# Kernel tuning notes

Measured on AMD Instinct MI355X. Metric: run time of the kernel, lower is better.

## Reference

```python
import jax, jax.numpy as jnp
import numpy as np

B, TQ, TK, D = 16, 2048, 2048, 128


def setup_inputs() -> dict:
    key = jax.random.key(0)
    kq, kk, kv, km = jax.random.split(key, 4)
    query = jax.random.normal(kq, (B, TQ, D), dtype=jnp.float32)
    key_t = jax.random.normal(kk, (B, TK, D), dtype=jnp.float32)
    value = jax.random.normal(kv, (B, TK, D), dtype=jnp.float32)
    mask = (jax.random.uniform(km, (B, TQ, TK)) > 0.9).astype(jnp.float32)
    return {"query": query, "key": key_t, "value": value, "mask": mask}


def reference(query, key, value, mask):
    # score = Q K^T / sqrt(dk)
    dk = jnp.asarray(query.shape[-1], query.dtype)
    score = jnp.einsum("bqd,bkd->bqk", query, key) / jnp.sqrt(dk)
    score = score + mask * (-10000.0)
    # NOTE: original code applies softmax over axis=1 (the query axis),
    # not the usual last axis; reproduced faithfully.
    attn_weights = jax.nn.softmax(score, axis=1)
    context = jnp.einsum("bqk,bkv->bqv", attn_weights, value)
    return context, attn_weights
```

## Files before the change

kernel.cpp:

```cpp
#include <hip/hip_runtime.h>

typedef __attribute__((ext_vector_type(8))) short s8v;
typedef __attribute__((ext_vector_type(4))) float f4v;

constexpr int BN = 16;
constexpr int TQ = 2048;
constexpr int TK = 2048;
constexpr int DH = 128;

__device__ __forceinline__ unsigned short f2bf(float f) {
  unsigned int u = __float_as_uint(f);
  u += 0x7fffu + ((u >> 16) & 1u);
  return (unsigned short)(u >> 16);
}
__device__ __forceinline__ float bf2f(unsigned short h) {
  return __uint_as_float(((unsigned int)h) << 16);
}

union QKSH {
  struct {
    unsigned short qhi[128][40];
    unsigned short qlo[128][40];
    unsigned short khi[128][40];
    unsigned short klo[128][40];
  } s;
  unsigned short msk[128][132];
};

__global__ __launch_bounds__(256, 4) void qk_exp_kernel(
    const float* __restrict__ Q, const float* __restrict__ K,
    const float* __restrict__ Msk, float* __restrict__ P,
    float* __restrict__ Z)
{
  __shared__ QKSH sh;

  const int kb = blockIdx.x, qb = blockIdx.y, b = blockIdx.z;
  const int tid = threadIdx.x;
  const int wave = tid >> 6, lane = tid & 63;
  const int wr = wave >> 1, wc = wave & 1;
  const int quad = lane >> 4, l16 = lane & 15;

  f4v acc[4][4];
#pragma unroll
  for (int i = 0; i < 4; ++i)
#pragma unroll
    for (int j = 0; j < 4; ++j)
      acc[i][j] = (f4v){0.f, 0.f, 0.f, 0.f};

  const float* Qb = Q + ((size_t)b * TQ + (size_t)qb * 128) * DH;
  const float* Kb = K + ((size_t)b * TK + (size_t)kb * 128) * DH;

  for (int dc = 0; dc < DH; dc += 32) {
    __syncthreads();
#pragma unroll
    for (int i = 0; i < 4; ++i) {
      int idx = i * 256 + tid;
      int r = idx >> 3, c = (idx & 7) * 4;
      float4 qv = *(const float4*)(Qb + (size_t)r * DH + dc + c);
      float4 kv = *(const float4*)(Kb + (size_t)r * DH + dc + c);
      unsigned short h;
      h = f2bf(qv.x); sh.s.qhi[r][c+0] = h; sh.s.qlo[r][c+0] = f2bf(qv.x - bf2f(h));
      h = f2bf(qv.y); sh.s.qhi[r][c+1] = h; sh.s.qlo[r][c+1] = f2bf(qv.y - bf2f(h));
      h = f2bf(qv.z); sh.s.qhi[r][c+2] = h; sh.s.qlo[r][c+2] = f2bf(qv.z - bf2f(h));
      h = f2bf(qv.w); sh.s.qhi[r][c+3] = h; sh.s.qlo[r][c+3] = f2bf(qv.w - bf2f(h));
      h = f2bf(kv.x); sh.s.khi[r][c+0] = h; sh.s.klo[r][c+0] = f2bf(kv.x - bf2f(h));
      h = f2bf(kv.y); sh.s.khi[r][c+1] = h; sh.s.klo[r][c+1] = f2bf(kv.y - bf2f(h));
      h = f2bf(kv.z); sh.s.khi[r][c+2] = h; sh.s.klo[r][c+2] = f2bf(kv.z - bf2f(h));
      h = f2bf(kv.w); sh.s.khi[r][c+3] = h; sh.s.klo[r][c+3] = f2bf(kv.w - bf2f(h));
    }
    __syncthreads();

    s8v ah[4], al[4];
#pragma unroll
    for (int i = 0; i < 4; ++i) {
      ah[i] = *(const s8v*)&sh.s.qhi[wr*64 + i*16 + l16][quad*8];
      al[i] = *(const s8v*)&sh.s.qlo[wr*64 + i*16 + l16][quad*8];
    }
#pragma unroll
    for (int j = 0; j < 4; ++j) {
      s8v bh = *(const s8v*)&sh.s.khi[wc*64 + j*16 + l16][quad*8];
      s8v bl = *(const s8v*)&sh.s.klo[wc*64 + j*16 + l16][quad*8];
#pragma unroll
      for (int i = 0; i < 4; ++i) {
        acc[i][j] = __builtin_amdgcn_mfma_f32_16x16x32_bf16(ah[i], bh, acc[i][j], 0, 0, 0);
        acc[i][j] = __builtin_amdgcn_mfma_f32_16x16x32_bf16(al[i], bh, acc[i][j], 0, 0, 0);
        acc[i][j] = __builtin_amdgcn_mfma_f32_16x16x32_bf16(ah[i], bl, acc[i][j], 0, 0, 0);
      }
    }
  }

  __syncthreads();
  {
    const float* MB = Msk + ((size_t)b * TQ + (size_t)qb * 128) * TK + (size_t)kb * 128;
#pragma unroll
    for (int it = 0; it < 16; ++it) {
      int idx = it * 256 + tid;
      int r = idx >> 5, c = (idx & 31) * 4;
      float4 mv = *(const float4*)(MB + (size_t)r * TK + c);
      ushort4 mu;
      mu.x = (mv.x != 0.f); mu.y = (mv.y != 0.f);
      mu.z = (mv.z != 0.f); mu.w = (mv.w != 0.f);
      *(ushort4*)&sh.msk[r][c] = mu;
    }
  }
  __syncthreads();

  const float scale = 0.08838834764831845f;
  float csum[4] = {0.f, 0.f, 0.f, 0.f};
#pragma unroll
  for (int i = 0; i < 4; ++i) {
    int lr0 = wr * 64 + i * 16 + quad * 4;
#pragma unroll
    for (int r = 0; r < 4; ++r) {
      size_t rowoff = ((size_t)b * TQ + qb * 128 + lr0 + r) * TK + kb * 128 + wc * 64;
      const unsigned short* mrow = &sh.msk[lr0 + r][wc * 64];
#pragma unroll
      for (int j = 0; j < 4; ++j) {
        unsigned short m = mrow[j * 16 + l16];
        float p = m ? 0.f : __expf(acc[i][j][r] * scale);
        P[rowoff + j * 16 + l16] = p;
        csum[j] += p;
      }
    }
  }
#pragma unroll
  for (int j = 0; j < 4; ++j) {
    float v = csum[j];
    v += __shfl_xor(v, 16, 64);
    v += __shfl_xor(v, 32, 64);
    if (quad == 0)
      atomicAdd(&Z[b * TK + kb * 128 + wc * 64 + j * 16 + l16], v);
  }
}

__global__ __launch_bounds__(256) void vtrans_kernel(
    const float* __restrict__ V, unsigned short* __restrict__ Vthi,
    unsigned short* __restrict__ Vtlo)
{
  __shared__ float tile[64][65];
  const int k0 = blockIdx.x * 64, d0 = blockIdx.y * 64, b = blockIdx.z;
  const int tid = threadIdx.x;
#pragma unroll
  for (int i = 0; i < 4; ++i) {
    int idx = i * 256 + tid;
    int r = idx >> 4, c = (idx & 15) * 4;
    float4 v = *(const float4*)(V + ((size_t)b * TK + k0 + r) * DH + d0 + c);
    tile[r][c] = v.x; tile[r][c+1] = v.y; tile[r][c+2] = v.z; tile[r][c+3] = v.w;
  }
  __syncthreads();
  const int dr = tid >> 2, kq = (tid & 3) * 16;
  size_t base = ((size_t)b * DH + d0 + dr) * TK + k0 + kq;
  unsigned short hbuf[16], lbuf[16];
#pragma unroll
  for (int j = 0; j < 16; ++j) {
    float f = tile[kq + j][dr];
    unsigned short h = f2bf(f);
    hbuf[j] = h;
    lbuf[j] = f2bf(f - bf2f(h));
  }
#pragma unroll
  for (int m = 0; m < 4; ++m) {
    ushort4 hv = make_ushort4(hbuf[4*m], hbuf[4*m+1], hbuf[4*m+2], hbuf[4*m+3]);
    ushort4 lv = make_ushort4(lbuf[4*m], lbuf[4*m+1], lbuf[4*m+2], lbuf[4*m+3]);
    *(ushort4*)(Vthi + base + 4*m) = hv;
    *(ushort4*)(Vtlo + base + 4*m) = lv;
  }
}

__global__ __launch_bounds__(256) void rz_kernel(const float* __restrict__ Z,
                                                 float* __restrict__ Rz) {
  int i = blockIdx.x * 256 + threadIdx.x;
  Rz[i] = 1.0f / Z[i];
}

union __align__(16) AVSH {
  struct {
    unsigned short a[64][40];
    unsigned short vh[128][40];
    unsigned short vl[128][40];
  } b[2];
  float ctx[64][131];
};

__global__ __launch_bounds__(256) void av_kernel(
    float* __restrict__ Attn, const unsigned short* __restrict__ Vthi,
    const unsigned short* __restrict__ Vtlo, const float* __restrict__ Rz,
    float* __restrict__ Ctx)
{
  __shared__ AVSH sh;
  const int qb = blockIdx.x, b = blockIdx.y;
  const int tid = threadIdx.x;
  const int wave = tid >> 6, lane = tid & 63;
  const int wr = wave >> 1, wc = wave & 1;
  const int quad = lane >> 4, l16 = lane & 15;

  f4v acc[4][2];
#pragma unroll
  for (int i = 0; i < 4; ++i)
#pragma unroll
    for (int j = 0; j < 2; ++j)
      acc[i][j] = (f4v){0.f, 0.f, 0.f, 0.f};

  float* attnB = Attn + ((size_t)b * TQ + (size_t)qb * 64) * TK;
  const unsigned short* vhB = Vthi + (size_t)b * DH * TK;
  const unsigned short* vlB = Vtlo + (size_t)b * DH * TK;
  const float* rzB = Rz + (size_t)b * TK;

  const int pc = (tid & 7) * 4;
  const int pr = tid >> 3;
  const int vc = (tid & 3) * 8;
  const int vr = tid >> 2;

  float4 pv0, pv1, rzv;
  uint4 vh0, vh1, vl0, vl1;

  auto load_chunk = [&](int kc) {
    pv0 = *(const float4*)(attnB + (size_t)pr * TK + kc + pc);
    pv1 = *(const float4*)(attnB + (size_t)(pr + 32) * TK + kc + pc);
    rzv = *(const float4*)(rzB + kc + pc);
    vh0 = *(const uint4*)(vhB + (size_t)vr * TK + kc + vc);
    vh1 = *(const uint4*)(vhB + (size_t)(vr + 64) * TK + kc + vc);
    vl0 = *(const uint4*)(vlB + (size_t)vr * TK + kc + vc);
    vl1 = *(const uint4*)(vlB + (size_t)(vr + 64) * TK + kc + vc);
  };

  auto stage_chunk = [&](int kc, int B) {
    float4 a0, a1;
    a0.x = pv0.x * rzv.x; a0.y = pv0.y * rzv.y;
    a0.z = pv0.z * rzv.z; a0.w = pv0.w * rzv.w;
    a1.x = pv1.x * rzv.x; a1.y = pv1.y * rzv.y;
    a1.z = pv1.z * rzv.z; a1.w = pv1.w * rzv.w;
    *(float4*)(attnB + (size_t)pr * TK + kc + pc) = a0;
    *(float4*)(attnB + (size_t)(pr + 32) * TK + kc + pc) = a1;
    *(ushort4*)&sh.b[B].a[pr][pc] =
        make_ushort4(f2bf(a0.x), f2bf(a0.y), f2bf(a0.z), f2bf(a0.w));
    *(ushort4*)&sh.b[B].a[pr + 32][pc] =
        make_ushort4(f2bf(a1.x), f2bf(a1.y), f2bf(a1.z), f2bf(a1.w));
    *(uint4*)&sh.b[B].vh[vr][vc] = vh0;
    *(uint4*)&sh.b[B].vh[vr + 64][vc] = vh1;
    *(uint4*)&sh.b[B].vl[vr][vc] = vl0;
    *(uint4*)&sh.b[B].vl[vr + 64][vc] = vl1;
  };

  load_chunk(0);
  stage_chunk(0, 0);
  __syncthreads();

  int cur = 0;
  constexpr int NT = TK / 32;
  for (int t = 0; t < NT; ++t) {
    if (t + 1 < NT) load_chunk((t + 1) * 32);

    s8v vhf[4], vlf[4], pf[2];
#pragma unroll
    for (int i = 0; i < 4; ++i) {
      vhf[i] = *(const s8v*)&sh.b[cur].vh[wr * 64 + i * 16 + l16][quad * 8];
      vlf[i] = *(const s8v*)&sh.b[cur].vl[wr * 64 + i * 16 + l16][quad * 8];
    }
#pragma unroll
    for (int j = 0; j < 2; ++j)
      pf[j] = *(const s8v*)&sh.b[cur].a[wc * 32 + j * 16 + l16][quad * 8];

#pragma unroll
    for (int i = 0; i < 4; ++i)
#pragma unroll
      for (int j = 0; j < 2; ++j) {
        acc[i][j] = __builtin_amdgcn_mfma_f32_16x16x32_bf16(vhf[i], pf[j], acc[i][j], 0, 0, 0);
        acc[i][j] = __builtin_amdgcn_mfma_f32_16x16x32_bf16(vlf[i], pf[j], acc[i][j], 0, 0, 0);
      }

    if (t + 1 < NT) {
      stage_chunk((t + 1) * 32, cur ^ 1);
      __syncthreads();
      cur ^= 1;
    }
  }

  __syncthreads();
#pragma unroll
  for (int i = 0; i < 4; ++i)
#pragma unroll
    for (int j = 0; j < 2; ++j)
#pragma unroll
      for (int r = 0; r < 4; ++r)
        sh.ctx[wc * 32 + j * 16 + l16][wr * 64 + i * 16 + quad * 4 + r] = acc[i][j][r];
  __syncthreads();
#pragma unroll
  for (int it = 0; it < 8; ++it) {
    int idx = it * 256 + tid;
    int r = idx >> 5, c = (idx & 31) * 4;
    float4 v;
    v.x = sh.ctx[r][c];     v.y = sh.ctx[r][c + 1];
    v.z = sh.ctx[r][c + 2]; v.w = sh.ctx[r][c + 3];
    *(float4*)(Ctx + ((size_t)b * TQ + qb * 64 + r) * DH + c) = v;
  }
}

extern "C" void kernel_launch(void* const* d_in, const int* in_sizes, int n_in,
                              void* d_out, int out_size, void* d_ws, size_t ws_size,
                              hipStream_t stream)
{
  const float* Q = (const float*)d_in[0];
  const float* K = (const float*)d_in[1];
  const float* V = (const float*)d_in[2];
  const float* M = (const float*)d_in[3];

  float* ctx  = (float*)d_out;
  float* attn = ctx + (size_t)BN * TQ * DH;

  char* ws = (char*)d_ws;
  float* Z  = (float*)ws;
  float* Rz = (float*)(ws + (128 << 10));
  unsigned short* Vthi = (unsigned short*)(ws + (1 << 20));
  unsigned short* Vtlo = Vthi + (size_t)BN * DH * TK;

  hipMemsetAsync(Z, 0, (size_t)BN * TK * sizeof(float), stream);
  vtrans_kernel<<<dim3(TK/64, DH/64, BN), 256, 0, stream>>>(V, Vthi, Vtlo);
  qk_exp_kernel<<<dim3(TK/128, TQ/128, BN), 256, 0, stream>>>(Q, K, M, attn, Z);
  rz_kernel<<<dim3((BN*TK)/256), 256, 0, stream>>>(Z, Rz);
  av_kernel<<<dim3(TQ/64, BN), 256, 0, stream>>>(attn, Vthi, Vtlo, Rz, ctx);
}
```

Baseline: 710.3 us.

## Store unnormalized scores as bf16 intermediate and fold normalization into V

```diff
diff --git a/kernel.cpp b/kernel.cpp
--- a/kernel.cpp
+++ b/kernel.cpp
@@ -27,10 +27,11 @@
   unsigned short msk[128][132];
 };
 
+template<int PB16>
 __global__ __launch_bounds__(256, 4) void qk_exp_kernel(
     const float* __restrict__ Q, const float* __restrict__ K,
     const float* __restrict__ Msk, float* __restrict__ P,
-    float* __restrict__ Z)
+    unsigned short* __restrict__ Pb, float* __restrict__ Z)
 {
   __shared__ QKSH sh;
 
@@ -118,7 +119,10 @@
       for (int j = 0; j < 4; ++j) {
         unsigned short m = mrow[j * 16 + l16];
         float p = m ? 0.f : __expf(acc[i][j][r] * scale);
-        P[rowoff + j * 16 + l16] = p;
+        if constexpr (PB16)
+          Pb[rowoff + j * 16 + l16] = f2bf(p);
+        else
+          P[rowoff + j * 16 + l16] = p;
         csum[j] += p;
       }
     }
@@ -133,9 +137,10 @@
   }
 }
 
+template<bool SCALE>
 __global__ __launch_bounds__(256) void vtrans_kernel(
-    const float* __restrict__ V, unsigned short* __restrict__ Vthi,
-    unsigned short* __restrict__ Vtlo)
+    const float* __restrict__ V, const float* __restrict__ Rz,
+    unsigned short* __restrict__ Vthi, unsigned short* __restrict__ Vtlo)
 {
   __shared__ float tile[64][65];
   const int k0 = blockIdx.x * 64, d0 = blockIdx.y * 64, b = blockIdx.z;
@@ -149,11 +154,20 @@
   }
   __syncthreads();
   const int dr = tid >> 2, kq = (tid & 3) * 16;
+  float rzbuf[16];
+  if constexpr (SCALE) {
+#pragma unroll
+    for (int m = 0; m < 4; ++m) {
+      float4 rv = *(const float4*)(Rz + (size_t)b * TK + k0 + kq + 4 * m);
+      rzbuf[4*m] = rv.x; rzbuf[4*m+1] = rv.y; rzbuf[4*m+2] = rv.z; rzbuf[4*m+3] = rv.w;
+    }
+  }
   size_t base = ((size_t)b * DH + d0 + dr) * TK + k0 + kq;
   unsigned short hbuf[16], lbuf[16];
 #pragma unroll
   for (int j = 0; j < 16; ++j) {
     float f = tile[kq + j][dr];
+    if constexpr (SCALE) f *= rzbuf[j];
     unsigned short h = f2bf(f);
     hbuf[j] = h;
     lbuf[j] = f2bf(f - bf2f(h));
@@ -182,7 +196,122 @@
   float ctx[64][131];
 };
 
-__global__ __launch_bounds__(256) void av_kernel(
+__global__ __launch_bounds__(256) void av_kernel_b(
+    const unsigned short* __restrict__ Pb, float* __restrict__ Attn,
+    const unsigned short* __restrict__ Vthi, const unsigned short* __restrict__ Vtlo,
+    const float* __restrict__ Rz, float* __restrict__ Ctx)
+{
+  __shared__ AVSH sh;
+  const int qb = blockIdx.x, b = blockIdx.y;
+  const int tid = threadIdx.x;
+  const int wave = tid >> 6, lane = tid & 63;
+  const int wr = wave >> 1, wc = wave & 1;
+  const int quad = lane >> 4, l16 = lane & 15;
+
+  f4v acc[4][2];
+#pragma unroll
+  for (int i = 0; i < 4; ++i)
+#pragma unroll
+    for (int j = 0; j < 2; ++j)
+      acc[i][j] = (f4v){0.f, 0.f, 0.f, 0.f};
+
+  const unsigned short* pbB = Pb + ((size_t)b * TQ + (size_t)qb * 64) * TK;
+  float* attnB = Attn + ((size_t)b * TQ + (size_t)qb * 64) * TK;
+  const unsigned short* vhB = Vthi + (size_t)b * DH * TK;
+  const unsigned short* vlB = Vtlo + (size_t)b * DH * TK;
+  const float* rzB = Rz + (size_t)b * TK;
+
+  const int ar = tid >> 2, ac = (tid & 3) * 8;
+  const int vr = tid >> 2, vc = (tid & 3) * 8;
+
+  s8v pa;
+  float4 rz0, rz1;
+  uint4 vh0, vh1, vl0, vl1;
+
+  auto load_chunk = [&](int kc) {
+    pa  = *(const s8v*)(pbB + (size_t)ar * TK + kc + ac);
+    rz0 = *(const float4*)(rzB + kc + ac);
+    rz1 = *(const float4*)(rzB + kc + ac + 4);
+    vh0 = *(const uint4*)(vhB + (size_t)vr * TK + kc + vc);
+    vh1 = *(const uint4*)(vhB + (size_t)(vr + 64) * TK + kc + vc);
+    vl0 = *(const uint4*)(vlB + (size_t)vr * TK + kc + vc);
+    vl1 = *(const uint4*)(vlB + (size_t)(vr + 64) * TK + kc + vc);
+  };
+
+  auto stage_chunk = [&](int kc, int B) {
+    float4 w0, w1;
+    w0.x = bf2f((unsigned short)pa[0]) * rz0.x;
+    w0.y = bf2f((unsigned short)pa[1]) * rz0.y;
+    w0.z = bf2f((unsigned short)pa[2]) * rz0.z;
+    w0.w = bf2f((unsigned short)pa[3]) * rz0.w;
+    w1.x = bf2f((unsigned short)pa[4]) * rz1.x;
+    w1.y = bf2f((unsigned short)pa[5]) * rz1.y;
+    w1.z = bf2f((unsigned short)pa[6]) * rz1.z;
+    w1.w = bf2f((unsigned short)pa[7]) * rz1.w;
+    *(float4*)(attnB + (size_t)ar * TK + kc + ac) = w0;
+    *(float4*)(attnB + (size_t)ar * TK + kc + ac + 4) = w1;
+    *(s8v*)&sh.b[B].a[ar][ac] = pa;
+    *(uint4*)&sh.b[B].vh[vr][vc] = vh0;
+    *(uint4*)&sh.b[B].vh[vr + 64][vc] = vh1;
+    *(uint4*)&sh.b[B].vl[vr][vc] = vl0;
+    *(uint4*)&sh.b[B].vl[vr + 64][vc] = vl1;
+  };
+
+  load_chunk(0);
+  stage_chunk(0, 0);
+  __syncthreads();
+
+  int cur = 0;
+  constexpr int NT = TK / 32;
+  for (int t = 0; t < NT; ++t) {
+    if (t + 1 < NT) load_chunk((t + 1) * 32);
+
+    s8v vhf[4], vlf[4], pf[2];
+#pragma unroll
+    for (int i = 0; i < 4; ++i) {
+      vhf[i] = *(const s8v*)&sh.b[cur].vh[wr * 64 + i * 16 + l16][quad * 8];
+      vlf[i] = *(const s8v*)&sh.b[cur].vl[wr * 64 + i * 16 + l16][quad * 8];
+    }
+#pragma unroll
+    for (int j = 0; j < 2; ++j)
+      pf[j] = *(const s8v*)&sh.b[cur].a[wc * 32 + j * 16 + l16][quad * 8];
+
+#pragma unroll
+    for (int i = 0; i < 4; ++i)
+#pragma unroll
+      for (int j = 0; j < 2; ++j) {
+        acc[i][j] = __builtin_amdgcn_mfma_f32_16x16x32_bf16(vhf[i], pf[j], acc[i][j], 0, 0, 0);
+        acc[i][j] = __builtin_amdgcn_mfma_f32_16x16x32_bf16(vlf[i], pf[j], acc[i][j], 0, 0, 0);
+      }
+
+    if (t + 1 < NT) {
+      stage_chunk((t + 1) * 32, cur ^ 1);
+      __syncthreads();
+      cur ^= 1;
+    }
+  }
+
+  __syncthreads();
+#pragma unroll
+  for (int i = 0; i < 4; ++i)
+#pragma unroll
+    for (int j = 0; j < 2; ++j)
+#pragma unroll
+      for (int r = 0; r < 4; ++r)
+        sh.ctx[wc * 32 + j * 16 + l16][wr * 64 + i * 16 + quad * 4 + r] = acc[i][j][r];
+  __syncthreads();
+#pragma unroll
+  for (int it = 0; it < 8; ++it) {
+    int idx = it * 256 + tid;
+    int r = idx >> 5, c = (idx & 31) * 4;
+    float4 v;
+    v.x = sh.ctx[r][c];     v.y = sh.ctx[r][c + 1];
+    v.z = sh.ctx[r][c + 2]; v.w = sh.ctx[r][c + 3];
+    *(float4*)(Ctx + ((size_t)b * TQ + qb * 64 + r) * DH + c) = v;
+  }
+}
+
+__global__ __launch_bounds__(256) void av_kernel_f(
     float* __restrict__ Attn, const unsigned short* __restrict__ Vthi,
     const unsigned short* __restrict__ Vtlo, const float* __restrict__ Rz,
     float* __restrict__ Ctx)
@@ -309,14 +438,31 @@
   float* attn = ctx + (size_t)BN * TQ * DH;
 
   char* ws = (char*)d_ws;
-  float* Z  = (float*)ws;
-  float* Rz = (float*)(ws + (128 << 10));
-  unsigned short* Vthi = (unsigned short*)(ws + (1 << 20));
-  unsigned short* Vtlo = Vthi + (size_t)BN * DH * TK;
-
-  hipMemsetAsync(Z, 0, (size_t)BN * TK * sizeof(float), stream);
-  vtrans_kernel<<<dim3(TK/64, DH/64, BN), 256, 0, stream>>>(V, Vthi, Vtlo);
-  qk_exp_kernel<<<dim3(TK/128, TQ/128, BN), 256, 0, stream>>>(Q, K, M, attn, Z);
-  rz_kernel<<<dim3((BN*TK)/256), 256, 0, stream>>>(Z, Rz);
-  av_kernel<<<dim3(TQ/64, BN), 256, 0, stream>>>(attn, Vthi, Vtlo, Rz, ctx);
-}
+  const size_t pbBytes = (size_t)BN * TQ * TK * 2;
+  const size_t bigNeed = (19ull << 20) + pbBytes;
+
+  if (ws_size >= bigNeed) {
+    float* Z  = (float*)ws;
+    float* Rz = (float*)(ws + (512 << 10));
+    unsigned short* Vthi = (unsigned short*)(ws + (1u << 20));
+    unsigned short* Vtlo = (unsigned short*)(ws + (10u << 20));
+    unsigned short* Pb   = (unsigned short*)(ws + (19u << 20));
+
+    hipMemsetAsync(Z, 0, (size_t)BN * TK * sizeof(float), stream);
+    qk_exp_kernel<1><<<dim3(TK/128, TQ/128, BN), 256, 0, stream>>>(Q, K, M, nullptr, Pb, Z);
+    rz_kernel<<<dim3((BN*TK)/256), 256, 0, stream>>>(Z, Rz);
+    vtrans_kernel<true><<<dim3(TK/64, DH/64, BN), 256, 0, stream>>>(V, Rz, Vthi, Vtlo);
+    av_kernel_b<<<dim3(TQ/64, BN), 256, 0, stream>>>(Pb, attn, Vthi, Vtlo, Rz, ctx);
+  } else {
+    float* Z  = (float*)ws;
+    float* Rz = (float*)(ws + (128 << 10));
+    unsigned short* Vthi = (unsigned short*)(ws + (1u << 20));
+    unsigned short* Vtlo = Vthi + (size_t)BN * DH * TK;
+
+    hipMemsetAsync(Z, 0, (size_t)BN * TK * sizeof(float), stream);
+    vtrans_kernel<false><<<dim3(TK/64, DH/64, BN), 256, 0, stream>>>(V, nullptr, Vthi, Vtlo);
+    qk_exp_kernel<0><<<dim3(TK/128, TQ/128, BN), 256, 0, stream>>>(Q, K, M, attn, nullptr, Z);
+    rz_kernel<<<dim3((BN*TK)/256), 256, 0, stream>>>(Z, Rz);
+    av_kernel_f<<<dim3(TQ/64, BN), 256, 0, stream>>>(attn, Vthi, Vtlo, Rz, ctx);
+  }
+}
```

New measurement: 660.9 us. -7.0%, faster.

## Store unnormalized probabilities as bf16 and fold column normalization into V

Applied to the files above, without the earlier changes.

```diff
diff --git a/kernel.cpp b/kernel.cpp
--- a/kernel.cpp
+++ b/kernel.cpp
@@ -27,9 +27,9 @@
   unsigned short msk[128][132];
 };
 
-__global__ __launch_bounds__(256, 4) void qk_exp_kernel(
+__global__ __launch_bounds__(256, 3) void qk_exp_kernel(
     const float* __restrict__ Q, const float* __restrict__ K,
-    const float* __restrict__ Msk, float* __restrict__ P,
+    const float* __restrict__ Msk, unsigned short* __restrict__ Pb,
     float* __restrict__ Z)
 {
   __shared__ QKSH sh;
@@ -49,8 +49,13 @@
 
   const float* Qb = Q + ((size_t)b * TQ + (size_t)qb * 128) * DH;
   const float* Kb = K + ((size_t)b * TK + (size_t)kb * 128) * DH;
-
-  for (int dc = 0; dc < DH; dc += 32) {
+  const float* MB = Msk + ((size_t)b * TQ + (size_t)qb * 128) * TK + (size_t)kb * 128;
+
+  ushort4 mu[16];
+
+#pragma unroll
+  for (int ch = 0; ch < 4; ++ch) {
+    const int dc = ch * 32;
     __syncthreads();
 #pragma unroll
     for (int i = 0; i < 4; ++i) {
@@ -70,6 +75,14 @@
     }
     __syncthreads();
 
+    float4 mld[4];
+#pragma unroll
+    for (int t = 0; t < 4; ++t) {
+      int idx = (ch * 4 + t) * 256 + tid;
+      int r = idx >> 5, c = (idx & 31) * 4;
+      mld[t] = *(const float4*)(MB + (size_t)r * TK + c);
+    }
+
     s8v ah[4], al[4];
 #pragma unroll
     for (int i = 0; i < 4; ++i) {
@@ -87,21 +100,20 @@
         acc[i][j] = __builtin_amdgcn_mfma_f32_16x16x32_bf16(ah[i], bl, acc[i][j], 0, 0, 0);
       }
     }
-  }
-
-  __syncthreads();
-  {
-    const float* MB = Msk + ((size_t)b * TQ + (size_t)qb * 128) * TK + (size_t)kb * 128;
-#pragma unroll
-    for (int it = 0; it < 16; ++it) {
-      int idx = it * 256 + tid;
-      int r = idx >> 5, c = (idx & 31) * 4;
-      float4 mv = *(const float4*)(MB + (size_t)r * TK + c);
-      ushort4 mu;
-      mu.x = (mv.x != 0.f); mu.y = (mv.y != 0.f);
-      mu.z = (mv.z != 0.f); mu.w = (mv.w != 0.f);
-      *(ushort4*)&sh.msk[r][c] = mu;
-    }
+
+#pragma unroll
+    for (int t = 0; t < 4; ++t) {
+      mu[ch * 4 + t] = make_ushort4(mld[t].x != 0.f, mld[t].y != 0.f,
+                                    mld[t].z != 0.f, mld[t].w != 0.f);
+    }
+  }
+
+  __syncthreads();
+#pragma unroll
+  for (int t = 0; t < 16; ++t) {
+    int idx = t * 256 + tid;
+    int r = idx >> 5, c = (idx & 31) * 4;
+    *(ushort4*)&sh.msk[r][c] = mu[t];
   }
   __syncthreads();
 
@@ -118,7 +130,7 @@
       for (int j = 0; j < 4; ++j) {
         unsigned short m = mrow[j * 16 + l16];
         float p = m ? 0.f : __expf(acc[i][j][r] * scale);
-        P[rowoff + j * 16 + l16] = p;
+        Pb[rowoff + j * 16 + l16] = f2bf(p);
         csum[j] += p;
       }
     }
@@ -134,8 +146,8 @@
 }
 
 __global__ __launch_bounds__(256) void vtrans_kernel(
-    const float* __restrict__ V, unsigned short* __restrict__ Vthi,
-    unsigned short* __restrict__ Vtlo)
+    const float* __restrict__ V, const float* __restrict__ Rz,
+    unsigned short* __restrict__ Vthi, unsigned short* __restrict__ Vtlo)
 {
   __shared__ float tile[64][65];
   const int k0 = blockIdx.x * 64, d0 = blockIdx.y * 64, b = blockIdx.z;
@@ -149,11 +161,17 @@
   }
   __syncthreads();
   const int dr = tid >> 2, kq = (tid & 3) * 16;
+  float rzbuf[16];
+#pragma unroll
+  for (int m = 0; m < 4; ++m) {
+    float4 rv = *(const float4*)(Rz + (size_t)b * TK + k0 + kq + 4 * m);
+    rzbuf[4*m] = rv.x; rzbuf[4*m+1] = rv.y; rzbuf[4*m+2] = rv.z; rzbuf[4*m+3] = rv.w;
+  }
   size_t base = ((size_t)b * DH + d0 + dr) * TK + k0 + kq;
   unsigned short hbuf[16], lbuf[16];
 #pragma unroll
   for (int j = 0; j < 16; ++j) {
-    float f = tile[kq + j][dr];
+    float f = tile[kq + j][dr] * rzbuf[j];
     unsigned short h = f2bf(f);
     hbuf[j] = h;
     lbuf[j] = f2bf(f - bf2f(h));
@@ -182,10 +200,10 @@
   float ctx[64][131];
 };
 
-__global__ __launch_bounds__(256) void av_kernel(
-    float* __restrict__ Attn, const unsigned short* __restrict__ Vthi,
-    const unsigned short* __restrict__ Vtlo, const float* __restrict__ Rz,
-    float* __restrict__ Ctx)
+__global__ __launch_bounds__(256) void av_kernel_b(
+    const unsigned short* __restrict__ Pb, float* __restrict__ Attn,
+    const unsigned short* __restrict__ Vthi, const unsigned short* __restrict__ Vtlo,
+    const float* __restrict__ Rz, float* __restrict__ Ctx)
 {
   __shared__ AVSH sh;
   const int qb = blockIdx.x, b = blockIdx.y;
@@ -201,23 +219,23 @@
     for (int j = 0; j < 2; ++j)
       acc[i][j] = (f4v){0.f, 0.f, 0.f, 0.f};
 
+  const unsigned short* pbB = Pb + ((size_t)b * TQ + (size_t)qb * 64) * TK;
   float* attnB = Attn + ((size_t)b * TQ + (size_t)qb * 64) * TK;
   const unsigned short* vhB = Vthi + (size_t)b * DH * TK;
   const unsigned short* vlB = Vtlo + (size_t)b * DH * TK;
   const float* rzB = Rz + (size_t)b * TK;
 
-  const int pc = (tid & 7) * 4;
-  const int pr = tid >> 3;
-  const int vc = (tid & 3) * 8;
-  const int vr = tid >> 2;
-
-  float4 pv0, pv1, rzv;
+  const int ar = tid >> 2, ac = (tid & 3) * 8;
+  const int vr = tid >> 2, vc = (tid & 3) * 8;
+
+  s8v pa;
+  float4 rz0, rz1;
   uint4 vh0, vh1, vl0, vl1;
 
   auto load_chunk = [&](int kc) {
-    pv0 = *(const float4*)(attnB + (size_t)pr * TK + kc + pc);
-    pv1 = *(const float4*)(attnB + (size_t)(pr + 32) * TK + kc + pc);
-    rzv = *(const float4*)(rzB + kc + pc);
+    pa  = *(const s8v*)(pbB + (size_t)ar * TK + kc + ac);
+    rz0 = *(const float4*)(rzB + kc + ac);
+    rz1 = *(const float4*)(rzB + kc + ac + 4);
     vh0 = *(const uint4*)(vhB + (size_t)vr * TK + kc + vc);
     vh1 = *(const uint4*)(vhB + (size_t)(vr + 64) * TK + kc + vc);
     vl0 = *(const uint4*)(vlB + (size_t)vr * TK + kc + vc);
@@ -225,17 +243,18 @@
   };
 
   auto stage_chunk = [&](int kc, int B) {
-    float4 a0, a1;
-    a0.x = pv0.x * rzv.x; a0.y = pv0.y * rzv.y;
-    a0.z = pv0.z * rzv.z; a0.w = pv0.w * rzv.w;
-    a1.x = pv1.x * rzv.x; a1.y = pv1.y * rzv.y;
-    a1.z = pv1.z * rzv.z; a1.w = pv1.w * rzv.w;
-    *(float4*)(attnB + (size_t)pr * TK + kc + pc) = a0;
-    *(float4*)(attnB + (size_t)(pr + 32) * TK + kc + pc) = a1;
-    *(ushort4*)&sh.b[B].a[pr][pc] =
-        make_ushort4(f2bf(a0.x), f2bf(a0.y), f2bf(a0.z), f2bf(a0.w));
-    *(ushort4*)&sh.b[B].a[pr + 32][pc] =
-        make_ushort4(f2bf(a1.x), f2bf(a1.y), f2bf(a1.z), f2bf(a1.w));
+    float4 w0, w1;
+    w0.x = bf2f((unsigned short)pa[0]) * rz0.x;
+    w0.y = bf2f((unsigned short)pa[1]) * rz0.y;
+    w0.z = bf2f((unsigned short)pa[2]) * rz0.z;
+    w0.w = bf2f((unsigned short)pa[3]) * rz0.w;
+    w1.x = bf2f((unsigned short)pa[4]) * rz1.x;
+    w1.y = bf2f((unsigned short)pa[5]) * rz1.y;
+    w1.z = bf2f((unsigned short)pa[6]) * rz1.z;
+    w1.w = bf2f((unsigned short)pa[7]) * rz1.w;
+    *(float4*)(attnB + (size_t)ar * TK + kc + ac) = w0;
+    *(float4*)(attnB + (size_t)ar * TK + kc + ac + 4) = w1;
+    *(s8v*)&sh.b[B].a[ar][ac] = pa;
     *(uint4*)&sh.b[B].vh[vr][vc] = vh0;
     *(uint4*)&sh.b[B].vh[vr + 64][vc] = vh1;
     *(uint4*)&sh.b[B].vl[vr][vc] = vl0;
@@ -310,13 +329,14 @@
 
   char* ws = (char*)d_ws;
   float* Z  = (float*)ws;
-  float* Rz = (float*)(ws + (128 << 10));
-  unsigned short* Vthi = (unsigned short*)(ws + (1 << 20));
-  unsigned short* Vtlo = Vthi + (size_t)BN * DH * TK;
+  float* Rz = (float*)(ws + (512 << 10));
+  unsigned short* Vthi = (unsigned short*)(ws + (1u << 20));
+  unsigned short* Vtlo = (unsigned short*)(ws + (10u << 20));
+  unsigned short* Pb   = (unsigned short*)(ws + (19u << 20));
 
   hipMemsetAsync(Z, 0, (size_t)BN * TK * sizeof(float), stream);
-  vtrans_kernel<<<dim3(TK/64, DH/64, BN), 256, 0, stream>>>(V, Vthi, Vtlo);
-  qk_exp_kernel<<<dim3(TK/128, TQ/128, BN), 256, 0, stream>>>(Q, K, M, attn, Z);
+  qk_exp_kernel<<<dim3(TK/128, TQ/128, BN), 256, 0, stream>>>(Q, K, M, Pb, Z);
   rz_kernel<<<dim3((BN*TK)/256), 256, 0, stream>>>(Z, Rz);
-  av_kernel<<<dim3(TQ/64, BN), 256, 0, stream>>>(attn, Vthi, Vtlo, Rz, ctx);
-}
+  vtrans_kernel<<<dim3(TK/64, DH/64, BN), 256, 0, stream>>>(V, Rz, Vthi, Vtlo);
+  av_kernel_b<<<dim3(TQ/64, BN), 256, 0, stream>>>(Pb, attn, Vthi, Vtlo, Rz, ctx);
+}
```

New measurement: 656.1 us. 1.08x faster.
